# Kernel tuning notes

Measured on AMD Instinct MI355X. Metric: run time of the kernel, lower is better.

The kernel has to match this reference:

```python
import jax, jax.numpy as jnp
import numpy as np

B, I, H = 16384, 512, 512


def setup_inputs() -> dict:
    key = jax.random.key(0)
    ks = jax.random.split(key, 9)
    std = 1.0 / np.sqrt(H)
    u = lambda k, shape: jax.random.uniform(k, shape, jnp.float32, -std, std)
    return {
        "input": jax.random.normal(ks[0], (B, I), jnp.float32),
        "h_prev": jax.random.normal(ks[1], (B, H), jnp.float32),
        "c_prev": jax.random.normal(ks[2], (B, H), jnp.float32),
        "m_prev": jax.random.normal(ks[3], (B, H), jnp.float32),
        "n_prev": jnp.ones((B, H), jnp.float32),
        "Wxh": u(ks[4], (4 * H, I)),
        "bxh": u(ks[5], (4 * H,)),
        "Whh": u(ks[6], (4 * H, H)),
        "bhh": u(ks[7], (4 * H,)),
    }


def reference(input, h_prev, c_prev, m_prev, n_prev, Wxh, bxh, Whh, bhh):
    # gates = xh(input) + hh(h_prev) -> [B, 4H]
    gates = input @ Wxh.T + bxh + h_prev @ Whh.T + bhh
    ig, fg, zg, og = jnp.split(gates, 4, axis=1)
    z_t = jnp.tanh(zg)
    o_t = jax.nn.sigmoid(og)
    # log-space stabilizer: log(exp(fg)) = fg, log(exp(ig)) = ig
    m_t = jnp.maximum(fg + m_prev, ig)
    i_t = jnp.exp(ig - m_t)
    f_t = jnp.exp(fg + m_prev - m_t)
    c_t = f_t * c_prev + i_t * z_t
    n_t = f_t * n_prev + i_t
    h_t = o_t * (c_t / n_t)
    return (h_t, c_t, m_t, n_t)
```

## Files before the change

### kernel.cpp

```cpp
#include <hip/hip_runtime.h>

#define Bsz 16384
#define Isz 512
#define Hsz 512
#define Ksz 1024
#define N4H 2048

#define BM 256
#define BN 256
#define BK 64

typedef __bf16 bf16x8 __attribute__((ext_vector_type(8)));
typedef __bf16 bf16x4 __attribute__((ext_vector_type(4)));
typedef float  f32x4  __attribute__((ext_vector_type(4)));

__device__ __forceinline__ void async_copy16(const void* g, void* l) {
    __builtin_amdgcn_global_load_lds(
        (__attribute__((address_space(1))) void*)g,
        (__attribute__((address_space(3))) void*)l,
        16, 0, 0);
}

__global__ void pack_all(const float* __restrict__ x, const float* __restrict__ h,
                         const float* __restrict__ Wxh, const float* __restrict__ Whh,
                         const float* __restrict__ bxh, const float* __restrict__ bhh,
                         __bf16* __restrict__ Aq, __bf16* __restrict__ Bq,
                         float* __restrict__ bias) {
    if (blockIdx.x < 16384) {
        int idx = blockIdx.x * 256 + threadIdx.x;
        int e   = idx << 2;
        int row = e >> 10, col = e & 1023;
        const float4 v = (col < Isz)
            ? *(const float4*)(x + (size_t)row * Isz + col)
            : *(const float4*)(h + (size_t)row * Hsz + (col - Isz));
        bf16x4 o = { (__bf16)v.x, (__bf16)v.y, (__bf16)v.z, (__bf16)v.w };
        *(bf16x4*)(Aq + (size_t)e) = o;
    } else {
        int idx = (blockIdx.x - 16384) * 256 + threadIdx.x;
        int p   = idx >> 8;
        int k   = (idx & 255) << 2;
        int nb  = p >> 7, n = p & 127;
        int wn  = n >> 6, t = (n >> 4) & 3, c = n & 15;
        int orow = t * Hsz + nb * 32 + wn * 16 + c;
        const float4 v = (k < Isz)
            ? *(const float4*)(Wxh + (size_t)orow * Isz + k)
            : *(const float4*)(Whh + (size_t)orow * Hsz + (k - Isz));
        bf16x4 o = { (__bf16)v.x, (__bf16)v.y, (__bf16)v.z, (__bf16)v.w };
        *(bf16x4*)(Bq + (size_t)p * Ksz + k) = o;
        if ((idx & 255) == 0) bias[p] = bxh[orow] + bhh[orow];
    }
}

#define CFENCE asm volatile("" ::: "memory")
#define BARRIER { CFENCE; __builtin_amdgcn_s_barrier(); CFENCE; }
#define WAITLGKM { asm volatile("s_waitcnt lgkmcnt(0)" ::: "memory"); \
                   __builtin_amdgcn_sched_barrier(0); }
#define WAITVM4  asm volatile("s_waitcnt vmcnt(4)" ::: "memory")

#define LDSA(p) ((unsigned)(size_t)(const __bf16 __attribute__((address_space(3)))*)(p))

#define DSR(dst, addr, IMM) \
    asm volatile("ds_read_b128 %0, %1 offset:" IMM : "=v"(dst) : "v"(addr))

#define LDS_A_(ap, I0, I1, I2, I3) { \
    const unsigned a0_ = LDSA((ap) + ko0), a1_ = LDSA((ap) + ko1); \
    DSR(af[0][0], a0_, I0); DSR(af[0][1], a1_, I0); \
    DSR(af[1][0], a0_, I1); DSR(af[1][1], a1_, I1); \
    DSR(af[2][0], a0_, I2); DSR(af[2][1], a1_, I2); \
    DSR(af[3][0], a0_, I3); DSR(af[3][1], a1_, I3); }
#define LDS_A0(ap) LDS_A_(ap, "0", "2048", "4096", "6144")
#define LDS_A4(ap) LDS_A_(ap, "8192", "10240", "12288", "14336")

#define LDS_B0(bp) { \
    const unsigned b0_ = LDSA((bp) + ko0), b1_ = LDSA((bp) + ko1); \
    DSR(bf[0][0], b0_, "0");    DSR(bf[0][1], b1_, "0"); \
    DSR(bf[1][0], b0_, "2048"); DSR(bf[1][1], b1_, "2048"); }
#define LDS_B2(bp) { \
    const unsigned b0_ = LDSA((bp) + ko0), b1_ = LDSA((bp) + ko1); \
    DSR(bf[2][0], b0_, "4096"); DSR(bf[2][1], b1_, "4096"); \
    DSR(bf[3][0], b0_, "6144"); DSR(bf[3][1], b1_, "6144"); }

#define MMA(fbase, nbase)                                                     \
    __builtin_amdgcn_s_setprio(1);                                            \
    _Pragma("unroll") for (int f = 0; f < 4; ++f)                             \
    _Pragma("unroll") for (int n = 0; n < 2; ++n)                             \
    _Pragma("unroll") for (int kk = 0; kk < 2; ++kk)                          \
        acc[(fbase) + f][(nbase) + n] = __builtin_amdgcn_mfma_f32_16x16x32_bf16( \
            af[f][kk], bf[(nbase) + n][kk], acc[(fbase) + f][(nbase) + n], 0, 0, 0); \
    __builtin_amdgcn_s_setprio(0);

#define STAGE(dst, src, half, step)                                           \
    { async_copy16((src) + (size_t)((half) * 128 + rrow) * Ksz + (step) * 64 + scol, \
                   (char*)(dst) + (half) * 16384 + tid * 16);                 \
      async_copy16((src) + (size_t)((half) * 128 + 64 + rrow) * Ksz + (step) * 64 + scol, \
                   (char*)(dst) + (half) * 16384 + 8192 + tid * 16); }

__global__ __launch_bounds__(512, 2) void slstm_gemm(
    const __bf16* __restrict__ Aq, const __bf16* __restrict__ Bq,
    const float* __restrict__ bias,
    const float* __restrict__ c_prev, const float* __restrict__ m_prev,
    const float* __restrict__ n_prev, float* __restrict__ out) {

    __shared__ __bf16 As0[BM * BK];
    __shared__ __bf16 As1[BM * BK];
    __shared__ __bf16 Bs0[BN * BK];
    __shared__ __bf16 Bs1[BN * BK];

    const int tid  = threadIdx.x;
    const int w    = tid >> 6;
    const int lane = tid & 63;
    const int wm   = w & 1;
    const int wc   = w >> 1;

    const int bm  = blockIdx.x;
    const int nbb = blockIdx.y;

    const int lr = lane & 15;
    const int g0 = lane >> 4;
    const int px = lr & 7;

    const __bf16* Ag = Aq + (size_t)bm  * BM * Ksz;
    const __bf16* Bg = Bq + (size_t)nbb * BN * Ksz;

    const int rrow = tid >> 3;
    const int scol = ((tid & 7) ^ (rrow & 7)) * 8;

    const __bf16* A0p = &As0[(wm * 128 + lr) * 64];
    const __bf16* A1p = &As1[(wm * 128 + lr) * 64];
    const __bf16* B0p = &Bs0[(wc * 64 + lr) * 64];
    const __bf16* B1p = &Bs1[(wc * 64 + lr) * 64];
    const int ko0 = ((0 * 4 + g0) ^ px) * 8;
    const int ko1 = ((1 * 4 + g0) ^ px) * 8;

    f32x4 acc[8][4];
    const f32x4 zero = {0.f, 0.f, 0.f, 0.f};
#pragma unroll
    for (int mi = 0; mi < 8; ++mi)
#pragma unroll
        for (int ni = 0; ni < 4; ++ni) acc[mi][ni] = zero;

    STAGE(Bs0, Bg, 0, 0);
    STAGE(Bs0, Bg, 1, 0);
    STAGE(As0, Ag, 0, 0);
    STAGE(As0, Ag, 1, 0);
    STAGE(Bs1, Bg, 0, 1);
    STAGE(Bs1, Bg, 1, 1);
    WAITVM4;
    BARRIER;

    bf16x8 af[4][2];
    bf16x8 bf[4][2];

#pragma unroll 1
    for (int i = 0; i < 8; ++i) {
        const int ic  = (i < 7) ? i : 6;
        const int sA1 = 2 * i + 1;
        const int sB0 = 2 * ic + 2;
        const int sB1 = 2 * ic + 3;

        LDS_A0(A0p);
        LDS_B0(B0p);
        STAGE(As1, Ag, 0, sA1);
        BARRIER; WAITLGKM;
        MMA(0, 0);
        BARRIER;

        LDS_B2(B0p);
        STAGE(As1, Ag, 1, sA1);
        BARRIER; WAITLGKM;
        MMA(0, 2);
        BARRIER;

        LDS_A4(A0p);
        STAGE(Bs0, Bg, 0, sB0);
        BARRIER; WAITLGKM;
        MMA(4, 2);
        BARRIER;

        STAGE(Bs0, Bg, 1, sB0);
        BARRIER;
        MMA(4, 0);
        WAITVM4;
        BARRIER;

        LDS_A0(A1p);
        LDS_B0(B1p);
        STAGE(As0, Ag, 0, sB0);
        BARRIER; WAITLGKM;
        MMA(0, 0);
        BARRIER;

        LDS_B2(B1p);
        STAGE(As0, Ag, 1, sB0);
        BARRIER; WAITLGKM;
        MMA(0, 2);
        BARRIER;

        LDS_A4(A1p);
        STAGE(Bs1, Bg, 0, sB1);
        BARRIER; WAITLGKM;
        MMA(4, 2);
        BARRIER;

        STAGE(Bs1, Bg, 1, sB1);
        BARRIER;
        MMA(4, 0);
        WAITVM4;
        BARRIER;
    }

    const int hidx = (nbb * 2 + (wc >> 1)) * 32 + (wc & 1) * 16 + lr;

    float bsv[4];
#pragma unroll
    for (int n = 0; n < 4; ++n)
        bsv[n] = bias[nbb * 256 + wc * 64 + n * 16 + lr];

    const size_t BH = (size_t)Bsz * Hsz;
    const float L2E  = 1.44269504089f;
    const float L2E2 = 2.88539008178f;

#pragma unroll
    for (int mi = 0; mi < 8; ++mi) {
        const int mbase = bm * 256 + wm * 128 + mi * 16 + g0 * 4;
#pragma unroll
        for (int r = 0; r < 4; ++r) {
            const int m = mbase + r;
            const size_t off = (size_t)m * Hsz + hidx;
            const float ig = acc[mi][0][r] + bsv[0];
            const float fg = acc[mi][1][r] + bsv[1];
            const float zg = acc[mi][2][r] + bsv[2];
            const float og = acc[mi][3][r] + bsv[3];
            const float cp = c_prev[off];
            const float mp = m_prev[off];
            const float np = n_prev[off];
            const float zt = 1.f - 2.f * __builtin_amdgcn_rcpf(
                                 __builtin_amdgcn_exp2f(zg * L2E2) + 1.f);
            const float ot = __builtin_amdgcn_rcpf(
                                 __builtin_amdgcn_exp2f(-og * L2E) + 1.f);
            const float fm = fg + mp;
            const float mt = fmaxf(fm, ig);
            const float it = __builtin_amdgcn_exp2f((ig - mt) * L2E);
            const float ft = __builtin_amdgcn_exp2f((fm - mt) * L2E);
            const float ct = ft * cp + it * zt;
            const float nt = ft * np + it;
            const float ht = ot * ct * __builtin_amdgcn_rcpf(nt);
            out[off]          = ht;
            out[BH + off]     = ct;
            out[2 * BH + off] = mt;
            out[3 * BH + off] = nt;
        }
    }
}

extern "C" void kernel_launch(void* const* d_in, const int* in_sizes, int n_in,
                              void* d_out, int out_size, void* d_ws, size_t ws_size,
                              hipStream_t stream) {
    const float* input  = (const float*)d_in[0];
    const float* h_prev = (const float*)d_in[1];
    const float* c_prev = (const float*)d_in[2];
    const float* m_prev = (const float*)d_in[3];
    const float* n_prev = (const float*)d_in[4];
    const float* Wxh    = (const float*)d_in[5];
    const float* bxh    = (const float*)d_in[6];
    const float* Whh    = (const float*)d_in[7];
    const float* bhh    = (const float*)d_in[8];
    float* out = (float*)d_out;

    __bf16* Aq   = (__bf16*)d_ws;
    __bf16* Bq   = (__bf16*)((char*)d_ws + (size_t)Bsz * Ksz * 2);
    float*  bias = (float*)((char*)d_ws + (size_t)Bsz * Ksz * 2 + (size_t)N4H * Ksz * 2);

    pack_all<<<16384 + 2048, 256, 0, stream>>>(input, h_prev, Wxh, Whh, bxh, bhh,
                                               Aq, Bq, bias);

    dim3 grid(Bsz / BM, N4H / BN);
    slstm_gemm<<<grid, 512, 0, stream>>>(Aq, Bq, bias, c_prev, m_prev, n_prev, out);
}
```

Baseline: 329.0 us.

## Halve K-tile to 32 and double occupancy with new LDS swizzle layout

Shrinks the K tile from 64 to 32 so each LDS buffer is half as big, and raises the launch-bounds occupancy hint from 2 to 4 blocks per CU. The staging and ds_read addressing is rebuilt with a new XOR swizzle for 64-byte rows packed two per 128-byte line. The K loop now runs 16 iterations with one MFMA per fragment pair instead of two. Higher occupancy is meant to hide latency better, at the cost of more barriers per unit of work and register pressure under the tighter bounds.

```diff
diff --git a/kernel.cpp b/kernel.cpp
--- a/kernel.cpp
+++ b/kernel.cpp
@@ -8,7 +8,7 @@
 
 #define BM 256
 #define BN 256
-#define BK 64
+#define BK 32
 
 typedef __bf16 bf16x8 __attribute__((ext_vector_type(8)));
 typedef __bf16 bf16x4 __attribute__((ext_vector_type(4)));
@@ -62,40 +62,26 @@
 #define DSR(dst, addr, IMM) \
     asm volatile("ds_read_b128 %0, %1 offset:" IMM : "=v"(dst) : "v"(addr))
 
-#define LDS_A_(ap, I0, I1, I2, I3) { \
-    const unsigned a0_ = LDSA((ap) + ko0), a1_ = LDSA((ap) + ko1); \
-    DSR(af[0][0], a0_, I0); DSR(af[0][1], a1_, I0); \
-    DSR(af[1][0], a0_, I1); DSR(af[1][1], a1_, I1); \
-    DSR(af[2][0], a0_, I2); DSR(af[2][1], a1_, I2); \
-    DSR(af[3][0], a0_, I3); DSR(af[3][1], a1_, I3); }
-#define LDS_A0(ap) LDS_A_(ap, "0", "2048", "4096", "6144")
-#define LDS_A4(ap) LDS_A_(ap, "8192", "10240", "12288", "14336")
-
-#define LDS_B0(bp) { \
-    const unsigned b0_ = LDSA((bp) + ko0), b1_ = LDSA((bp) + ko1); \
-    DSR(bf[0][0], b0_, "0");    DSR(bf[0][1], b1_, "0"); \
-    DSR(bf[1][0], b0_, "2048"); DSR(bf[1][1], b1_, "2048"); }
-#define LDS_B2(bp) { \
-    const unsigned b0_ = LDSA((bp) + ko0), b1_ = LDSA((bp) + ko1); \
-    DSR(bf[2][0], b0_, "4096"); DSR(bf[2][1], b1_, "4096"); \
-    DSR(bf[3][0], b0_, "6144"); DSR(bf[3][1], b1_, "6144"); }
-
-#define MMA(fbase, nbase)                                                     \
+#define LDS_A03(ab) { DSR(af[0], ab, "0");    DSR(af[1], ab, "1024"); \
+                      DSR(af[2], ab, "2048"); DSR(af[3], ab, "3072"); }
+#define LDS_A47(ab) { DSR(af[4], ab, "4096"); DSR(af[5], ab, "5120"); \
+                      DSR(af[6], ab, "6144"); DSR(af[7], ab, "7168"); }
+#define LDS_B01(bb) { DSR(bf[0], bb, "0");    DSR(bf[1], bb, "1024"); }
+#define LDS_B23(bb) { DSR(bf[2], bb, "2048"); DSR(bf[3], bb, "3072"); }
+
+#define MMA8(fb, nb)                                                          \
     __builtin_amdgcn_s_setprio(1);                                            \
     _Pragma("unroll") for (int f = 0; f < 4; ++f)                             \
     _Pragma("unroll") for (int n = 0; n < 2; ++n)                             \
-    _Pragma("unroll") for (int kk = 0; kk < 2; ++kk)                          \
-        acc[(fbase) + f][(nbase) + n] = __builtin_amdgcn_mfma_f32_16x16x32_bf16( \
-            af[f][kk], bf[(nbase) + n][kk], acc[(fbase) + f][(nbase) + n], 0, 0, 0); \
+        acc[(fb) + f][(nb) + n] = __builtin_amdgcn_mfma_f32_16x16x32_bf16(    \
+            af[(fb) + f], bf[(nb) + n], acc[(fb) + f][(nb) + n], 0, 0, 0);    \
     __builtin_amdgcn_s_setprio(0);
 
-#define STAGE(dst, src, half, step)                                           \
-    { async_copy16((src) + (size_t)((half) * 128 + rrow) * Ksz + (step) * 64 + scol, \
-                   (char*)(dst) + (half) * 16384 + tid * 16);                 \
-      async_copy16((src) + (size_t)((half) * 128 + 64 + rrow) * Ksz + (step) * 64 + scol, \
-                   (char*)(dst) + (half) * 16384 + 8192 + tid * 16); }
-
-__global__ __launch_bounds__(512, 2) void slstm_gemm(
+#define STAGE_H(dst, srcS, half, step)                                        \
+    async_copy16((srcS) + (size_t)(half) * 131072 + (step) * 32,              \
+                 (char*)(dst) + (half) * 8192 + tid * 16);
+
+__global__ __launch_bounds__(512, 4) void slstm_gemm(
     const __bf16* __restrict__ Aq, const __bf16* __restrict__ Bq,
     const float* __restrict__ bias,
     const float* __restrict__ c_prev, const float* __restrict__ m_prev,
@@ -117,20 +103,21 @@
 
     const int lr = lane & 15;
     const int g0 = lane >> 4;
-    const int px = lr & 7;
 
     const __bf16* Ag = Aq + (size_t)bm  * BM * Ksz;
     const __bf16* Bg = Bq + (size_t)nbb * BN * Ksz;
 
-    const int rrow = tid >> 3;
-    const int scol = ((tid & 7) ^ (rrow & 7)) * 8;
-
-    const __bf16* A0p = &As0[(wm * 128 + lr) * 64];
-    const __bf16* A1p = &As1[(wm * 128 + lr) * 64];
-    const __bf16* B0p = &Bs0[(wc * 64 + lr) * 64];
-    const __bf16* B1p = &Bs1[(wc * 64 + lr) * 64];
-    const int ko0 = ((0 * 4 + g0) ^ px) * 8;
-    const int ko1 = ((1 * 4 + g0) ^ px) * 8;
+    const int sgp  = (tid & 7) ^ ((tid >> 3) & 7);
+    const int sr0  = ((tid >> 3) << 1) + (sgp >> 2);
+    const int skc  = (sgp & 3) << 3;
+    const __bf16* AgS = Ag + (size_t)sr0 * Ksz + skc;
+    const __bf16* BgS = Bg + (size_t)sr0 * Ksz + skc;
+
+    const int p_rd = (((lr & 1) << 2) | g0) ^ ((lr >> 1) & 7);
+    const unsigned aoff = (unsigned)((wm * 64 + (lr >> 1)) * 128 + p_rd * 16);
+    const unsigned boff = (unsigned)((wc * 32 + (lr >> 1)) * 128 + p_rd * 16);
+    const unsigned a0b = LDSA(As0) + aoff, a1b = LDSA(As1) + aoff;
+    const unsigned b0b = LDSA(Bs0) + boff, b1b = LDSA(Bs1) + boff;
 
     f32x4 acc[8][4];
     const f32x4 zero = {0.f, 0.f, 0.f, 0.f};
@@ -139,72 +126,62 @@
 #pragma unroll
         for (int ni = 0; ni < 4; ++ni) acc[mi][ni] = zero;
 
-    STAGE(Bs0, Bg, 0, 0);
-    STAGE(Bs0, Bg, 1, 0);
-    STAGE(As0, Ag, 0, 0);
-    STAGE(As0, Ag, 1, 0);
-    STAGE(Bs1, Bg, 0, 1);
-    STAGE(Bs1, Bg, 1, 1);
+    STAGE_H(As0, AgS, 0, 0); STAGE_H(As0, AgS, 1, 0);
+    STAGE_H(Bs0, BgS, 0, 0); STAGE_H(Bs0, BgS, 1, 0);
+    STAGE_H(As1, AgS, 0, 1); STAGE_H(As1, AgS, 1, 1);
+    STAGE_H(Bs1, BgS, 0, 1); STAGE_H(Bs1, BgS, 1, 1);
     WAITVM4;
     BARRIER;
 
-    bf16x8 af[4][2];
-    bf16x8 bf[4][2];
+    bf16x8 af[8];
+    bf16x8 bf[4];
 
 #pragma unroll 1
-    for (int i = 0; i < 8; ++i) {
-        const int ic  = (i < 7) ? i : 6;
-        const int sA1 = 2 * i + 1;
-        const int sB0 = 2 * ic + 2;
-        const int sB1 = 2 * ic + 3;
-
-        LDS_A0(A0p);
-        LDS_B0(B0p);
-        STAGE(As1, Ag, 0, sA1);
-        BARRIER; WAITLGKM;
-        MMA(0, 0);
-        BARRIER;
-
-        LDS_B2(B0p);
-        STAGE(As1, Ag, 1, sA1);
-        BARRIER; WAITLGKM;
-        MMA(0, 2);
-        BARRIER;
-
-        LDS_A4(A0p);
-        STAGE(Bs0, Bg, 0, sB0);
-        BARRIER; WAITLGKM;
-        MMA(4, 2);
-        BARRIER;
-
-        STAGE(Bs0, Bg, 1, sB0);
-        BARRIER;
-        MMA(4, 0);
+    for (int it = 0; it < 16; ++it) {
+        const int t0 = (it < 15) ? 2 * it + 2 : 31;
+        const int t1 = (it < 15) ? 2 * it + 3 : 31;
+        __bf16* Ad0 = (it < 15) ? As0 : As1;
+        __bf16* Bd0 = (it < 15) ? Bs0 : Bs1;
+
+        LDS_A03(a0b); LDS_B01(b0b);
+        BARRIER; WAITLGKM;
+        MMA8(0, 0);
+        BARRIER;
+        LDS_B23(b0b);
+        BARRIER; WAITLGKM;
+        MMA8(0, 2);
+        BARRIER;
+        LDS_A47(a0b);
+        STAGE_H(Bd0, BgS, 0, t0);
+        BARRIER; WAITLGKM;
+        MMA8(4, 2);
+        BARRIER;
+        STAGE_H(Bd0, BgS, 1, t0);
+        STAGE_H(Ad0, AgS, 0, t0);
+        STAGE_H(Ad0, AgS, 1, t0);
+        BARRIER;
+        MMA8(4, 0);
         WAITVM4;
         BARRIER;
 
-        LDS_A0(A1p);
-        LDS_B0(B1p);
-        STAGE(As0, Ag, 0, sB0);
-        BARRIER; WAITLGKM;
-        MMA(0, 0);
-        BARRIER;
-
-        LDS_B2(B1p);
-        STAGE(As0, Ag, 1, sB0);
-        BARRIER; WAITLGKM;
-        MMA(0, 2);
-        BARRIER;
-
-        LDS_A4(A1p);
-        STAGE(Bs1, Bg, 0, sB1);
-        BARRIER; WAITLGKM;
-        MMA(4, 2);
-        BARRIER;
-
-        STAGE(Bs1, Bg, 1, sB1);
-        BARRIER;
-        MMA(4, 0);
+        LDS_A03(a1b); LDS_B01(b1b);
+        BARRIER; WAITLGKM;
+        MMA8(0, 0);
+        BARRIER;
+        LDS_B23(b1b);
+        BARRIER; WAITLGKM;
+        MMA8(0, 2);
+        BARRIER;
+        LDS_A47(a1b);
+        STAGE_H(Bs1, BgS, 0, t1);
+        BARRIER; WAITLGKM;
+        MMA8(4, 2);
+        BARRIER;
+        STAGE_H(Bs1, BgS, 1, t1);
+        STAGE_H(As1, AgS, 0, t1);
+        STAGE_H(As1, AgS, 1, t1);
+        BARRIER;
+        MMA8(4, 0);
         WAITVM4;
         BARRIER;
     }
@@ -240,10 +217,10 @@
                                  __builtin_amdgcn_exp2f(-og * L2E) + 1.f);
             const float fm = fg + mp;
             const float mt = fmaxf(fm, ig);
-            const float it = __builtin_amdgcn_exp2f((ig - mt) * L2E);
-            const float ft = __builtin_amdgcn_exp2f((fm - mt) * L2E);
-            const float ct = ft * cp + it * zt;
-            const float nt = ft * np + it;
+            const float it2 = __builtin_amdgcn_exp2f((ig - mt) * L2E);
+            const float ft  = __builtin_amdgcn_exp2f((fm - mt) * L2E);
+            const float ct = ft * cp + it2 * zt;
+            const float nt = ft * np + it2;
             const float ht = ot * ct * __builtin_amdgcn_rcpf(nt);
             out[off]          = ht;
             out[BH + off]     = ct;
```

Measured after the change: 923.8 us. 2.81x slower.
